# Optimization experiments

Measured on AMD Instinct MI355X. Metric: run time of the kernel, lower is better.

## Reference

```python
import jax, jax.numpy as jnp
import numpy as np

N_NODES = 20000
N_EDGES = 320000
IN_F = 256
OUT_F = 64
HEADS = 4
ALPHA = 0.1  # leaky_relu negative slope


def setup_inputs() -> dict:
    key = jax.random.key(0)
    ks = jax.random.split(key, 8)
    return {
        "input1": jax.random.normal(ks[0], (N_NODES, IN_F), jnp.float32),
        "input2": jax.random.normal(ks[1], (N_NODES, IN_F), jnp.float32),
        # per-head params: Ws maps source feats -> target_out, Wt maps target feats -> source_out
        "Ws": jax.random.normal(ks[2], (HEADS, IN_F, OUT_F), jnp.float32) * 0.06,
        "Wt": jax.random.normal(ks[3], (HEADS, IN_F, OUT_F), jnp.float32) * 0.06,
        "a1": jax.random.normal(ks[4], (HEADS, 2 * OUT_F), jnp.float32) * 0.1,
        "a2": jax.random.normal(ks[5], (HEADS, 2 * OUT_F), jnp.float32) * 0.1,
        # COO nonzeros of A_opt [n_target, n_source]
        "tgt_idx": jax.random.randint(ks[6], (N_EDGES,), 0, N_NODES),
        "src_idx": jax.random.randint(ks[7], (N_EDGES,), 0, N_NODES),
    }


def _segment_softmax(scores, seg, num_segments):
    m = jax.lax.stop_gradient(jax.ops.segment_max(scores, seg, num_segments=num_segments))
    w = jnp.exp(scores - m[seg])
    d = jax.ops.segment_sum(w, seg, num_segments=num_segments)
    d = jnp.where(d == 0, 1.0, d)
    return w / d[seg]


def _head(x1, x2, Ws, Wt, a1, a2, src, tgt, n_s, n_t):
    s = x1 @ Ws  # [n_s, OUT_F]  messages source -> target
    t = x2 @ Wt  # [n_t, OUT_F]  messages target -> source
    out = Ws.shape[1]
    # edge score e = leaky_relu(a^T [s_src || t_tgt]); split a to avoid edge-level concat
    e1 = jax.nn.leaky_relu((s @ a1[:out])[src] + (t @ a1[out:])[tgt], ALPHA)
    e2 = jax.nn.leaky_relu((s @ a2[:out])[src] + (t @ a2[out:])[tgt], ALPHA)
    alpha_ts = _segment_softmax(e1, tgt, n_t)  # softmax over sources per target
    alpha_st = _segment_softmax(e2, src, n_s)  # softmax over targets per source
    h_ts = jax.ops.segment_sum(alpha_ts[:, None] * s[src], tgt, num_segments=n_t)
    h_st = jax.ops.segment_sum(alpha_st[:, None] * t[tgt], src, num_segments=n_s)
    return jax.nn.elu(h_st), jax.nn.elu(h_ts)  # concat=True -> ELU per head


def reference(input1, input2, Ws, Wt, a1, a2, tgt_idx, src_idx):
    n_s, n_t = input1.shape[0], input2.shape[0]
    head_fn = jax.vmap(
        lambda W1, W2, v1, v2: _head(input1, input2, W1, W2, v1, v2, src_idx, tgt_idx, n_s, n_t)
    )
    h_st, h_ts = head_fn(Ws, Wt, a1, a2)  # each [H, n, OUT_F]
    h_st = jnp.transpose(h_st, (1, 0, 2)).reshape(n_s, -1)  # concat heads
    h_ts = jnp.transpose(h_ts, (1, 0, 2)).reshape(n_t, -1)
    return h_st, h_ts
```

## Files before the change

### kernel.cpp

```cpp
#include <hip/hip_runtime.h>
#include <math.h>

#define N_NODES 20000
#define N_EDGES 320000
#define IN_F 256
#define OUT_F 64
#define HEADS 4
#define NCOL 256
#define LRELU_ALPHA 0.1f
#define ELL_CAP 64

#define SCAT_BLOCKS 1250

#define GEMM_GB 157
#define AGG_BLOCKS 2048

typedef __attribute__((ext_vector_type(8))) short short8;
typedef __attribute__((ext_vector_type(4))) float floatx4;

__device__ __forceinline__ float lrelu(float x) {
    return x > 0.f ? x : LRELU_ALPHA * x;
}
__device__ __forceinline__ unsigned short f2bf(float f) {
    unsigned int u = __float_as_uint(f);
    u = (u + 0x7FFF + ((u >> 16) & 1)) >> 16;
    return (unsigned short)u;
}
__device__ __forceinline__ float bf2f(unsigned short u) {
    return __uint_as_float(((unsigned int)u) << 16);
}

__global__ __launch_bounds__(256) void prep_w_kernel(
    const float* __restrict__ Ws, const float* __restrict__ Wt,
    unsigned short* __restrict__ Wsb, unsigned short* __restrict__ Wtb,
    int* __restrict__ cnt)
{
    const int gid = blockIdx.x * 256 + threadIdx.x;

    for (int i = gid; i < 2 * N_NODES; i += 16384) cnt[i] = 0;

    const int mat = gid >> 13;
    const int r   = gid & 8191;
    const int kc  = r >> 8;
    const int c   = r & 255;
    const float* W    = mat ? Wt : Ws;
    unsigned short* O = mat ? Wtb : Wsb;
    const int h = c >> 6, j = c & 63;
    const int k0 = kc * 8;
    unsigned short v[8] __attribute__((aligned(16)));
#pragma unroll
    for (int i = 0; i < 8; ++i)
        v[i] = f2bf(W[(size_t)h * (IN_F * OUT_F) + (size_t)(k0 + i) * OUT_F + j]);
    *(uint4*)(O + (size_t)c * IN_F + k0) = *(const uint4*)v;
}

__global__ __launch_bounds__(256) void scatter_kernel(
    const int* __restrict__ src, const int* __restrict__ tgt,
    int* __restrict__ cnt_t, int* __restrict__ cnt_s,
    unsigned short* __restrict__ elist_t, unsigned short* __restrict__ elist_s)
{
    const int e = blockIdx.x * 256 + threadIdx.x;
    const int s = src[e], t = tgt[e];
    const int p = atomicAdd(&cnt_t[t], 1);
    const int q = atomicAdd(&cnt_s[s], 1);
    if (p < ELL_CAP) elist_t[t * ELL_CAP + p] = (unsigned short)s;
    if (q < ELL_CAP) elist_s[s * ELL_CAP + q] = (unsigned short)t;
}

__global__ __launch_bounds__(512, 4) void gemm_wres_kernel(
    const float* __restrict__ A0, const unsigned short* __restrict__ Wb0,
    const float* __restrict__ A1, const unsigned short* __restrict__ Wb1,
    unsigned short* __restrict__ C0, unsigned short* __restrict__ C1,
    const float* __restrict__ a1, const float* __restrict__ a2,
    float* __restrict__ ss1, float* __restrict__ ss2,
    float* __restrict__ tt1, float* __restrict__ tt2)
{
    const int tid  = threadIdx.x;
    const int half = blockIdx.x & 1;
    const int gb   = blockIdx.x >> 1;
    const float* A           = (blockIdx.y == 0) ? A0 : A1;
    const unsigned short* Wb = (blockIdx.y == 0) ? Wb0 : Wb1;
    unsigned short* C        = (blockIdx.y == 0) ? C0 : C1;

    __shared__ __align__(16) unsigned short Bl[128][264];

    for (int i = tid; i < 4096; i += 512) {
        const int n  = i >> 5;
        const int kc = (i & 31) << 3;
        *(uint4*)&Bl[n][kc] = *(const uint4*)(Wb + (size_t)(half * 128 + n) * IN_F + kc);
    }
    __syncthreads();

    const int lane = tid & 63;
    const int w    = tid >> 6;
    const int quad = lane >> 4;
    const int l15  = lane & 15;
    const int g    = gb * 8 + w;
    if (g >= 1250) return;

    const float* arow = A + (size_t)(g * 16 + l15) * IN_F + quad * 8;

    float4 ua[8];
#pragma unroll
    for (int kk = 0; kk < 4; ++kk) {
        ua[2 * kk]     = *(const float4*)(arow + kk * 32);
        ua[2 * kk + 1] = *(const float4*)(arow + kk * 32 + 4);
    }
    short8 af[4];
#pragma unroll
    for (int kk = 0; kk < 4; ++kk) {
        short8 t;
        t[0] = (short)f2bf(ua[2 * kk].x);     t[1] = (short)f2bf(ua[2 * kk].y);
        t[2] = (short)f2bf(ua[2 * kk].z);     t[3] = (short)f2bf(ua[2 * kk].w);
        t[4] = (short)f2bf(ua[2 * kk + 1].x); t[5] = (short)f2bf(ua[2 * kk + 1].y);
        t[6] = (short)f2bf(ua[2 * kk + 1].z); t[7] = (short)f2bf(ua[2 * kk + 1].w);
        af[kk] = t;
    }

    float4 ub[8];
#pragma unroll
    for (int kk = 0; kk < 4; ++kk) {
        ub[2 * kk]     = *(const float4*)(arow + (kk + 4) * 32);
        ub[2 * kk + 1] = *(const float4*)(arow + (kk + 4) * 32 + 4);
    }

    floatx4 acc[8];
#pragma unroll
    for (int c = 0; c < 8; ++c) acc[c] = (floatx4){0.f, 0.f, 0.f, 0.f};

#pragma unroll
    for (int kk = 0; kk < 4; ++kk) {
#pragma unroll
        for (int c = 0; c < 8; ++c) {
            short8 bfrag = *(const short8*)&Bl[c * 16 + l15][kk * 32 + quad * 8];
            acc[c] = __builtin_amdgcn_mfma_f32_16x16x32_bf16(af[kk], bfrag, acc[c], 0, 0, 0);
        }
    }

#pragma unroll
    for (int kk = 0; kk < 4; ++kk) {
        short8 t;
        t[0] = (short)f2bf(ub[2 * kk].x);     t[1] = (short)f2bf(ub[2 * kk].y);
        t[2] = (short)f2bf(ub[2 * kk].z);     t[3] = (short)f2bf(ub[2 * kk].w);
        t[4] = (short)f2bf(ub[2 * kk + 1].x); t[5] = (short)f2bf(ub[2 * kk + 1].y);
        t[6] = (short)f2bf(ub[2 * kk + 1].z); t[7] = (short)f2bf(ub[2 * kk + 1].w);
        af[kk] = t;
    }
#pragma unroll
    for (int kk = 0; kk < 4; ++kk) {
#pragma unroll
        for (int c = 0; c < 8; ++c) {
            short8 bfrag = *(const short8*)&Bl[c * 16 + l15][(kk + 4) * 32 + quad * 8];
            acc[c] = __builtin_amdgcn_mfma_f32_16x16x32_bf16(af[kk], bfrag, acc[c], 0, 0, 0);
        }
    }

#pragma unroll
    for (int c = 0; c < 8; ++c) {
        const int col = half * 128 + c * 16 + l15;
#pragma unroll
        for (int r = 0; r < 4; ++r) {
            const int m = g * 16 + quad * 4 + r;
            C[(size_t)m * NCOL + col] = f2bf(acc[c][r]);
        }
    }

    const int off_aj = (blockIdx.y == 0) ? 0 : 64;
    float* o1 = (blockIdx.y == 0) ? ss1 : tt1;
    float* o2 = (blockIdx.y == 0) ? ss2 : tt2;

    float p1[2][4] = {{0.f,0.f,0.f,0.f},{0.f,0.f,0.f,0.f}};
    float p2[2][4] = {{0.f,0.f,0.f,0.f},{0.f,0.f,0.f,0.f}};
#pragma unroll
    for (int c = 0; c < 8; ++c) {
        const int hl = c >> 2;
        const int hh = half * 2 + hl;
        const int jj = (c & 3) * 16 + l15;
        const float w1 = a1[hh * 128 + off_aj + jj];
        const float w2 = a2[hh * 128 + off_aj + jj];
#pragma unroll
        for (int r = 0; r < 4; ++r) {
            p1[hl][r] += acc[c][r] * w1;
            p2[hl][r] += acc[c][r] * w2;
        }
    }
#pragma unroll
    for (int m = 1; m < 16; m <<= 1) {
#pragma unroll
        for (int hl = 0; hl < 2; ++hl)
#pragma unroll
            for (int r = 0; r < 4; ++r) {
                p1[hl][r] += __shfl_xor(p1[hl][r], m, 64);
                p2[hl][r] += __shfl_xor(p2[hl][r], m, 64);
            }
    }
    if (l15 == 0) {
#pragma unroll
        for (int r = 0; r < 4; ++r) {
            const int m = g * 16 + quad * 4 + r;
#pragma unroll
            for (int hl = 0; hl < 2; ++hl) {
                const int hh = half * 2 + hl;
                o1[m * HEADS + hh] = p1[hl][r];
                o2[m * HEADS + hh] = p2[hl][r];
            }
        }
    }
}

__global__ __launch_bounds__(256) void agg_kernel(
    const int* __restrict__ cnt_t, const unsigned short* __restrict__ elist_t,
    const int* __restrict__ cnt_s, const unsigned short* __restrict__ elist_s,
    const float* __restrict__ ss1, const float* __restrict__ ss2,
    const float* __restrict__ tt1, const float* __restrict__ tt2,
    const unsigned short* __restrict__ s_bf, const unsigned short* __restrict__ t_bf,
    float* __restrict__ h_st, float* __restrict__ h_ts)
{
    const int b     = blockIdx.x;
    const int slice = b & 7;
    const int dir   = slice >> 2;
    const int h     = slice & 3;
    const int idx   = b >> 3;
    const int qg    = threadIdx.x >> 4;
    const int l15   = threadIdx.x & 15;
    const int coff  = h * 64 + l15 * 4;

    const int*            cnt   = dir ? cnt_s   : cnt_t;
    const unsigned short* list  = dir ? elist_s : elist_t;
    const unsigned short* table = dir ? t_bf    : s_bf;
    const float*          nsc   = dir ? ss2     : tt1;
    const float*          esc   = dir ? tt2     : ss1;
    float*                outp  = dir ? h_st    : h_ts;

    const float* esch = esc + h;

    const int nstart = (idx * N_NODES) >> 8;
    const int nend   = ((idx + 1) * N_NODES) >> 8;

    for (int n = nstart + qg; n < nend; n += 16) {
        const float base = nsc[n * HEADS + h];
        int deg = cnt[n];
        if (deg > ELL_CAP) deg = ELL_CAP;
        const unsigned short* lp = list + n * ELL_CAP;

        float4 acc = make_float4(0.f, 0.f, 0.f, 0.f);
        float den = 0.f;

        int p = 0;
        for (; p + 3 < deg; p += 4) {
            int m0 = lp[p],     m1 = lp[p + 1];
            int m2 = lp[p + 2], m3 = lp[p + 3];
            float e0 = esch[m0 * HEADS], e1 = esch[m1 * HEADS];
            float e2 = esch[m2 * HEADS], e3 = esch[m3 * HEADS];
            ushort4 r0 = *(const ushort4*)(table + (size_t)m0 * NCOL + coff);
            ushort4 r1 = *(const ushort4*)(table + (size_t)m1 * NCOL + coff);
            ushort4 r2 = *(const ushort4*)(table + (size_t)m2 * NCOL + coff);
            ushort4 r3 = *(const ushort4*)(table + (size_t)m3 * NCOL + coff);
            float w0 = __expf(lrelu(e0 + base));
            float w1 = __expf(lrelu(e1 + base));
            float w2 = __expf(lrelu(e2 + base));
            float w3 = __expf(lrelu(e3 + base));
            den += (w0 + w1) + (w2 + w3);
            acc.x += (w0 * bf2f(r0.x) + w1 * bf2f(r1.x)) + (w2 * bf2f(r2.x) + w3 * bf2f(r3.x));
            acc.y += (w0 * bf2f(r0.y) + w1 * bf2f(r1.y)) + (w2 * bf2f(r2.y) + w3 * bf2f(r3.y));
            acc.z += (w0 * bf2f(r0.z) + w1 * bf2f(r1.z)) + (w2 * bf2f(r2.z) + w3 * bf2f(r3.z));
            acc.w += (w0 * bf2f(r0.w) + w1 * bf2f(r1.w)) + (w2 * bf2f(r2.w) + w3 * bf2f(r3.w));
        }
        for (; p < deg; ++p) {
            int m0 = lp[p];
            float w0 = __expf(lrelu(esch[m0 * HEADS] + base));
            ushort4 r0 = *(const ushort4*)(table + (size_t)m0 * NCOL + coff);
            den += w0;
            acc.x += w0 * bf2f(r0.x);
            acc.y += w0 * bf2f(r0.y);
            acc.z += w0 * bf2f(r0.z);
            acc.w += w0 * bf2f(r0.w);
        }

        if (den == 0.f) den = 1.f;
        float inv = 1.f / den;
        float4 r;
        r.x = acc.x * inv; r.y = acc.y * inv;
        r.z = acc.z * inv; r.w = acc.w * inv;
        r.x = (r.x > 0.f) ? r.x : expm1f(r.x);
        r.y = (r.y > 0.f) ? r.y : expm1f(r.y);
        r.z = (r.z > 0.f) ? r.z : expm1f(r.z);
        r.w = (r.w > 0.f) ? r.w : expm1f(r.w);
        *(float4*)(outp + (size_t)n * NCOL + coff) = r;
    }
}

extern "C" void kernel_launch(void* const* d_in, const int* in_sizes, int n_in,
                              void* d_out, int out_size, void* d_ws, size_t ws_size,
                              hipStream_t stream)
{
    const float* input1 = (const float*)d_in[0];
    const float* input2 = (const float*)d_in[1];
    const float* Ws     = (const float*)d_in[2];
    const float* Wt     = (const float*)d_in[3];
    const float* a1     = (const float*)d_in[4];
    const float* a2     = (const float*)d_in[5];
    const int*   tgt    = (const int*)d_in[6];
    const int*   src    = (const int*)d_in[7];

    float* out  = (float*)d_out;
    float* h_st = out;
    float* h_ts = out + (size_t)N_NODES * NCOL;

    unsigned short* s_bf = (unsigned short*)d_ws;
    unsigned short* t_bf = s_bf + (size_t)N_NODES * NCOL;
    unsigned short* Wsb  = t_bf + (size_t)N_NODES * NCOL;
    unsigned short* Wtb  = Wsb + 256 * 256;
    float* ss1  = (float*)(Wtb + 256 * 256);
    float* ss2  = ss1 + N_NODES * HEADS;
    float* tt1  = ss2 + N_NODES * HEADS;
    float* tt2  = tt1 + N_NODES * HEADS;
    int*   cnt_t = (int*)(tt2 + N_NODES * HEADS);
    int*   cnt_s = cnt_t + N_NODES;
    unsigned short* elist_t = (unsigned short*)(cnt_s + N_NODES);
    unsigned short* elist_s = elist_t + (size_t)N_NODES * ELL_CAP;

    prep_w_kernel<<<64, 256, 0, stream>>>(Ws, Wt, Wsb, Wtb, cnt_t);

    scatter_kernel<<<SCAT_BLOCKS, 256, 0, stream>>>(src, tgt, cnt_t, cnt_s,
                                                    elist_t, elist_s);

    dim3 ggrid(GEMM_GB * 2, 2);
    gemm_wres_kernel<<<ggrid, 512, 0, stream>>>(input1, Wsb, input2, Wtb,
                                                s_bf, t_bf, a1, a2,
                                                ss1, ss2, tt1, tt2);

    agg_kernel<<<AGG_BLOCKS, 256, 0, stream>>>(cnt_t, elist_t, cnt_s, elist_s,
                                               ss1, ss2, tt1, tt2, s_bf, t_bf, h_st, h_ts);
}
```

Measured before the change: 205.5 us.

## Fuse edge scatter into GEMM launch and remap aggregation to one wave per node

The edge-list scatter is merged into the GEMM kernel as extra blocks in the same grid. Scatter and projection GEMM are independent, so they can run concurrently and one launch is saved. Aggregation changes from 16-lane groups looping over node ranges to one 64-lane wave per node covering all four heads, launched as 10000 blocks. This gives wider coalesced row gathers but duplicates the neighbor-list reads across head lanes. Scatter blocks also reserve the GEMM's large shared buffer, which may limit co-residency.

```diff
diff --git a/kernel.cpp b/kernel.cpp
--- a/kernel.cpp
+++ b/kernel.cpp
@@ -10,10 +10,8 @@
 #define LRELU_ALPHA 0.1f
 #define ELL_CAP 64
 
-#define SCAT_BLOCKS 1250
-
+#define SCAT_X 313
 #define GEMM_GB 157
-#define AGG_BLOCKS 2048
 
 typedef __attribute__((ext_vector_type(8))) short short8;
 typedef __attribute__((ext_vector_type(4))) float floatx4;
@@ -54,35 +52,39 @@
     *(uint4*)(O + (size_t)c * IN_F + k0) = *(const uint4*)v;
 }
 
-__global__ __launch_bounds__(256) void scatter_kernel(
-    const int* __restrict__ src, const int* __restrict__ tgt,
-    int* __restrict__ cnt_t, int* __restrict__ cnt_s,
-    unsigned short* __restrict__ elist_t, unsigned short* __restrict__ elist_s)
-{
-    const int e = blockIdx.x * 256 + threadIdx.x;
-    const int s = src[e], t = tgt[e];
-    const int p = atomicAdd(&cnt_t[t], 1);
-    const int q = atomicAdd(&cnt_s[s], 1);
-    if (p < ELL_CAP) elist_t[t * ELL_CAP + p] = (unsigned short)s;
-    if (q < ELL_CAP) elist_s[s * ELL_CAP + q] = (unsigned short)t;
-}
-
-__global__ __launch_bounds__(512, 4) void gemm_wres_kernel(
+__global__ __launch_bounds__(512, 4) void hybrid_kernel(
     const float* __restrict__ A0, const unsigned short* __restrict__ Wb0,
     const float* __restrict__ A1, const unsigned short* __restrict__ Wb1,
     unsigned short* __restrict__ C0, unsigned short* __restrict__ C1,
     const float* __restrict__ a1, const float* __restrict__ a2,
     float* __restrict__ ss1, float* __restrict__ ss2,
-    float* __restrict__ tt1, float* __restrict__ tt2)
+    float* __restrict__ tt1, float* __restrict__ tt2,
+    const int* __restrict__ src, const int* __restrict__ tgt,
+    int* __restrict__ cnt_t, int* __restrict__ cnt_s,
+    unsigned short* __restrict__ elist_t, unsigned short* __restrict__ elist_s)
 {
-    const int tid  = threadIdx.x;
-    const int half = blockIdx.x & 1;
-    const int gb   = blockIdx.x >> 1;
+    const int tid = threadIdx.x;
+
+    __shared__ __align__(16) unsigned short Bl[128][264];
+
+    if (blockIdx.x < SCAT_X) {
+        const int e = ((int)blockIdx.y * SCAT_X + (int)blockIdx.x) * 512 + tid;
+        if (e < N_EDGES) {
+            const int s = src[e], t = tgt[e];
+            const int p = atomicAdd(&cnt_t[t], 1);
+            const int q = atomicAdd(&cnt_s[s], 1);
+            if (p < ELL_CAP) elist_t[t * ELL_CAP + p] = (unsigned short)s;
+            if (q < ELL_CAP) elist_s[s * ELL_CAP + q] = (unsigned short)t;
+        }
+        return;
+    }
+
+    const int gx   = blockIdx.x - SCAT_X;
+    const int half = gx & 1;
+    const int gb   = gx >> 1;
     const float* A           = (blockIdx.y == 0) ? A0 : A1;
     const unsigned short* Wb = (blockIdx.y == 0) ? Wb0 : Wb1;
     unsigned short* C        = (blockIdx.y == 0) ? C0 : C1;
-
-    __shared__ __align__(16) unsigned short Bl[128][264];
 
     for (int i = tid; i < 4096; i += 512) {
         const int n  = i >> 5;
@@ -216,14 +218,13 @@
     const unsigned short* __restrict__ s_bf, const unsigned short* __restrict__ t_bf,
     float* __restrict__ h_st, float* __restrict__ h_ts)
 {
-    const int b     = blockIdx.x;
-    const int slice = b & 7;
-    const int dir   = slice >> 2;
-    const int h     = slice & 3;
-    const int idx   = b >> 3;
-    const int qg    = threadIdx.x >> 4;
-    const int l15   = threadIdx.x & 15;
-    const int coff  = h * 64 + l15 * 4;
+    const int b    = blockIdx.x;
+    const int dir  = b & 1;
+    const int wave = threadIdx.x >> 6;
+    const int lane = threadIdx.x & 63;
+    const int n    = (b >> 1) * 4 + wave;
+    const int h    = lane >> 4;
+    const int coff = lane * 4;
 
     const int*            cnt   = dir ? cnt_s   : cnt_t;
     const unsigned short* list  = dir ? elist_s : elist_t;
@@ -232,62 +233,54 @@
     const float*          esc   = dir ? tt2     : ss1;
     float*                outp  = dir ? h_st    : h_ts;
 
-    const float* esch = esc + h;
-
-    const int nstart = (idx * N_NODES) >> 8;
-    const int nend   = ((idx + 1) * N_NODES) >> 8;
-
-    for (int n = nstart + qg; n < nend; n += 16) {
-        const float base = nsc[n * HEADS + h];
-        int deg = cnt[n];
-        if (deg > ELL_CAP) deg = ELL_CAP;
-        const unsigned short* lp = list + n * ELL_CAP;
-
-        float4 acc = make_float4(0.f, 0.f, 0.f, 0.f);
-        float den = 0.f;
-
-        int p = 0;
-        for (; p + 3 < deg; p += 4) {
-            int m0 = lp[p],     m1 = lp[p + 1];
-            int m2 = lp[p + 2], m3 = lp[p + 3];
-            float e0 = esch[m0 * HEADS], e1 = esch[m1 * HEADS];
-            float e2 = esch[m2 * HEADS], e3 = esch[m3 * HEADS];
-            ushort4 r0 = *(const ushort4*)(table + (size_t)m0 * NCOL + coff);
-            ushort4 r1 = *(const ushort4*)(table + (size_t)m1 * NCOL + coff);
-            ushort4 r2 = *(const ushort4*)(table + (size_t)m2 * NCOL + coff);
-            ushort4 r3 = *(const ushort4*)(table + (size_t)m3 * NCOL + coff);
-            float w0 = __expf(lrelu(e0 + base));
-            float w1 = __expf(lrelu(e1 + base));
-            float w2 = __expf(lrelu(e2 + base));
-            float w3 = __expf(lrelu(e3 + base));
-            den += (w0 + w1) + (w2 + w3);
-            acc.x += (w0 * bf2f(r0.x) + w1 * bf2f(r1.x)) + (w2 * bf2f(r2.x) + w3 * bf2f(r3.x));
-            acc.y += (w0 * bf2f(r0.y) + w1 * bf2f(r1.y)) + (w2 * bf2f(r2.y) + w3 * bf2f(r3.y));
-            acc.z += (w0 * bf2f(r0.z) + w1 * bf2f(r1.z)) + (w2 * bf2f(r2.z) + w3 * bf2f(r3.z));
-            acc.w += (w0 * bf2f(r0.w) + w1 * bf2f(r1.w)) + (w2 * bf2f(r2.w) + w3 * bf2f(r3.w));
-        }
-        for (; p < deg; ++p) {
-            int m0 = lp[p];
-            float w0 = __expf(lrelu(esch[m0 * HEADS] + base));
-            ushort4 r0 = *(const ushort4*)(table + (size_t)m0 * NCOL + coff);
-            den += w0;
-            acc.x += w0 * bf2f(r0.x);
-            acc.y += w0 * bf2f(r0.y);
-            acc.z += w0 * bf2f(r0.z);
-            acc.w += w0 * bf2f(r0.w);
-        }
-
-        if (den == 0.f) den = 1.f;
-        float inv = 1.f / den;
-        float4 r;
-        r.x = acc.x * inv; r.y = acc.y * inv;
-        r.z = acc.z * inv; r.w = acc.w * inv;
-        r.x = (r.x > 0.f) ? r.x : expm1f(r.x);
-        r.y = (r.y > 0.f) ? r.y : expm1f(r.y);
-        r.z = (r.z > 0.f) ? r.z : expm1f(r.z);
-        r.w = (r.w > 0.f) ? r.w : expm1f(r.w);
-        *(float4*)(outp + (size_t)n * NCOL + coff) = r;
-    }
+    const float base = nsc[n * HEADS + h];
+    int deg = cnt[n];
+    if (deg > ELL_CAP) deg = ELL_CAP;
+    const int b0 = n * ELL_CAP, b1 = b0 + deg;
+
+    float4 acc = make_float4(0.f, 0.f, 0.f, 0.f);
+    float den = 0.f;
+
+    int p = b0;
+    for (; p + 3 < b1; p += 4) {
+        int m0 = list[p],     m1 = list[p + 1];
+        int m2 = list[p + 2], m3 = list[p + 3];
+        float e0 = esc[m0 * HEADS + h], e1 = esc[m1 * HEADS + h];
+        float e2 = esc[m2 * HEADS + h], e3 = esc[m3 * HEADS + h];
+        ushort4 r0 = *(const ushort4*)(table + (size_t)m0 * NCOL + coff);
+        ushort4 r1 = *(const ushort4*)(table + (size_t)m1 * NCOL + coff);
+        ushort4 r2 = *(const ushort4*)(table + (size_t)m2 * NCOL + coff);
+        ushort4 r3 = *(const ushort4*)(table + (size_t)m3 * NCOL + coff);
+        float w0 = __expf(lrelu(e0 + base));
+        float w1 = __expf(lrelu(e1 + base));
+        float w2 = __expf(lrelu(e2 + base));
+        float w3 = __expf(lrelu(e3 + base));
+        den += (w0 + w1) + (w2 + w3);
+        acc.x += (w0 * bf2f(r0.x) + w1 * bf2f(r1.x)) + (w2 * bf2f(r2.x) + w3 * bf2f(r3.x));
+        acc.y += (w0 * bf2f(r0.y) + w1 * bf2f(r1.y)) + (w2 * bf2f(r2.y) + w3 * bf2f(r3.y));
+        acc.z += (w0 * bf2f(r0.z) + w1 * bf2f(r1.z)) + (w2 * bf2f(r2.z) + w3 * bf2f(r3.z));
+        acc.w += (w0 * bf2f(r0.w) + w1 * bf2f(r1.w)) + (w2 * bf2f(r2.w) + w3 * bf2f(r3.w));
+    }
+    for (; p < b1; ++p) {
+        int m0 = list[p];
+        float w0 = __expf(lrelu(esc[m0 * HEADS + h] + base));
+        ushort4 r0 = *(const ushort4*)(table + (size_t)m0 * NCOL + coff);
+        den += w0;
+        acc.x += w0 * bf2f(r0.x);
+        acc.y += w0 * bf2f(r0.y);
+        acc.z += w0 * bf2f(r0.z);
+        acc.w += w0 * bf2f(r0.w);
+    }
+
+    if (den == 0.f) den = 1.f;
+    float inv = 1.f / den;
+    float4 r;
+    r.x = acc.x * inv; r.y = acc.y * inv; r.z = acc.z * inv; r.w = acc.w * inv;
+    r.x = (r.x > 0.f) ? r.x : expm1f(r.x);
+    r.y = (r.y > 0.f) ? r.y : expm1f(r.y);
+    r.z = (r.z > 0.f) ? r.z : expm1f(r.z);
+    r.w = (r.w > 0.f) ? r.w : expm1f(r.w);
+    *(float4*)(outp + (size_t)n * NCOL + coff) = r;
 }
 
 extern "C" void kernel_launch(void* const* d_in, const int* in_sizes, int n_in,
@@ -322,14 +315,13 @@
 
     prep_w_kernel<<<64, 256, 0, stream>>>(Ws, Wt, Wsb, Wtb, cnt_t);
 
-    scatter_kernel<<<SCAT_BLOCKS, 256, 0, stream>>>(src, tgt, cnt_t, cnt_s,
-                                                    elist_t, elist_s);
-
-    dim3 ggrid(GEMM_GB * 2, 2);
-    gemm_wres_kernel<<<ggrid, 512, 0, stream>>>(input1, Wsb, input2, Wtb,
-                                                s_bf, t_bf, a1, a2,
-                                                ss1, ss2, tt1, tt2);
-
-    agg_kernel<<<AGG_BLOCKS, 256, 0, stream>>>(cnt_t, elist_t, cnt_s, elist_s,
-                                               ss1, ss2, tt1, tt2, s_bf, t_bf, h_st, h_ts);
-}
+    dim3 ggrid(SCAT_X + GEMM_GB * 2, 2);
+    hybrid_kernel<<<ggrid, 512, 0, stream>>>(input1, Wsb, input2, Wtb,
+                                             s_bf, t_bf, a1, a2,
+                                             ss1, ss2, tt1, tt2,
+                                             src, tgt, cnt_t, cnt_s,
+                                             elist_t, elist_s);
+
+    agg_kernel<<<10000, 256, 0, stream>>>(cnt_t, elist_t, cnt_s, elist_s,
+                                          ss1, ss2, tt1, tt2, s_bf, t_bf, h_st, h_ts);
+}
```

After: 184.5 us. 1.11x faster.
